# Performance work log

Measured on AMD Instinct MI355X. Metric: run time of the kernel, lower is better.

Reference implementation:

```python
import jax, jax.numpy as jnp
import numpy as np

# NF4 codebook (16 values, as in bitsandbytes / torchao), block size 64
NF4_CODEBOOK = jnp.array([
    -1.0, -0.6961928009986877, -0.5250730514526367, -0.39491748809814453,
    -0.28444138169288635, -0.18477343022823334, -0.09105003625154495, 0.0,
    0.07958029955625534, 0.16093020141124725, 0.24611230194568634,
    0.33791524171829224, 0.44070982933044434, 0.5626170039176941,
    0.7229568362236023, 1.0], dtype=jnp.float32)
BLOCK = 64
IN_DIM, OUT_DIM, RANK, ALPHA = 4096, 4096, 16, 32.0
N_TOKENS = 8192


def setup_inputs() -> dict:
    key = jax.random.key(0)
    kw, kx, ka, kb = jax.random.split(key, 4)
    # full-precision weight, then NF4-quantize (per-block absmax scaler + nearest code)
    w = jax.random.normal(kw, (OUT_DIM, IN_DIM), dtype=jnp.float32) * 0.02
    blocks = w.reshape(-1, BLOCK)                                   # [n_blocks, 64]
    scalers = jnp.max(jnp.abs(blocks), axis=1) + 1e-12              # [n_blocks]
    normed = blocks / scalers[:, None]
    codes = jnp.argmin(jnp.abs(normed[:, :, None] - NF4_CODEBOOK[None, None, :]),
                       axis=-1).astype(jnp.int32)                   # [n_blocks, 64]
    x = jax.random.normal(kx, (N_TOKENS, IN_DIM), dtype=jnp.float32)
    # kaiming_uniform_(a=sqrt(5)) -> U(-1/sqrt(fan_in), 1/sqrt(fan_in))
    bound_a = 1.0 / np.sqrt(IN_DIM)
    bound_b = 1.0 / np.sqrt(RANK)
    lora_a_w = jax.random.uniform(ka, (RANK, IN_DIM), minval=-bound_a, maxval=bound_a, dtype=jnp.float32)
    lora_b_w = jax.random.uniform(kb, (OUT_DIM, RANK), minval=-bound_b, maxval=bound_b, dtype=jnp.float32)
    return {"x": x, "codes": codes, "scalers": scalers,
            "lora_a_w": lora_a_w, "lora_b_w": lora_b_w}


def reference(x, codes, scalers, lora_a_w, lora_b_w):
    in_dim = x.shape[-1]
    out_dim = (codes.shape[0] * codes.shape[1]) // in_dim
    # NF4 dequant: code -> codebook value, times per-block absmax scaler
    w = (NF4_CODEBOOK[codes] * scalers[:, None]).reshape(out_dim, in_dim)
    base = x @ w.T                                                  # [N, out_dim]
    # LoRA branch (dropout p=0.0 -> identity): (alpha/rank) * B(A(x))
    lora = (x @ lora_a_w.T) @ lora_b_w.T
    return base + (ALPHA / RANK) * lora
```

## Files before the change

kernel.cpp:

```cpp
#include <hip/hip_runtime.h>

#define IN_DIM 4096
#define OUT_DIM 4096
#define NTOK 8192
#define LORA_SCALE 2.0f

typedef __bf16 bf16x8 __attribute__((ext_vector_type(8)));
typedef float f32x4 __attribute__((ext_vector_type(4)));

__device__ __constant__ float NF4_CB[16] = {
    -1.0f, -0.6961928009986877f, -0.5250730514526367f, -0.39491748809814453f,
    -0.28444138169288635f, -0.18477343022823334f, -0.09105003625154495f, 0.0f,
    0.07958029955625534f, 0.16093020141124725f, 0.24611230194568634f,
    0.33791524171829224f, 0.44070982933044434f, 0.5626170039176941f,
    0.7229568362236023f, 1.0f};

#define GLOAD16(g, l)                                                         \
  __builtin_amdgcn_global_load_lds(                                           \
      (const __attribute__((address_space(1))) void*)(g),                     \
      (__attribute__((address_space(3))) void*)(l), 16, 0, 0)

#define WEFF2_BLOCKS (OUT_DIM / 8 * (IN_DIM / 2048))
#define XCVT_BLOCKS (NTOK * IN_DIM / (256 * 8))

__global__ __launch_bounds__(256) void prep_kernel(
    const float* __restrict__ x, const int* __restrict__ codes,
    const float* __restrict__ scalers, const float* __restrict__ la,
    const float* __restrict__ lb, __bf16* __restrict__ xb,
    __bf16* __restrict__ weff) {
  if (blockIdx.x < WEFF2_BLOCKS) {
    const int lane = threadIdx.x & 63;
    const float cbv = NF4_CB[lane & 15];
    const int o0 = (blockIdx.x >> 1) * 8;
    const int k = ((blockIdx.x & 1) << 11) + threadIdx.x * 8;
    float4 a[16][2];
#pragma unroll
    for (int r = 0; r < 16; ++r) {
      a[r][0] = *(const float4*)(la + r * IN_DIM + k);
      a[r][1] = *(const float4*)(la + r * IN_DIM + k + 4);
    }
#pragma unroll 1
    for (int rr = 0; rr < 8; ++rr) {
      const int o = o0 + rr;
      const size_t base = (size_t)o * IN_DIM + k;
      const float sc = scalers[base >> 6];
      const int4 c0 = *(const int4*)(codes + base);
      const int4 c1 = *(const int4*)(codes + base + 4);
      float v[8];
      v[0] = __shfl(cbv, c0.x, 64) * sc; v[1] = __shfl(cbv, c0.y, 64) * sc;
      v[2] = __shfl(cbv, c0.z, 64) * sc; v[3] = __shfl(cbv, c0.w, 64) * sc;
      v[4] = __shfl(cbv, c1.x, 64) * sc; v[5] = __shfl(cbv, c1.y, 64) * sc;
      v[6] = __shfl(cbv, c1.z, 64) * sc; v[7] = __shfl(cbv, c1.w, 64) * sc;
      const float* lbo = lb + o * 16;
#pragma unroll
      for (int r = 0; r < 16; ++r) {
        float br = LORA_SCALE * lbo[r];
        v[0] += br * a[r][0].x; v[1] += br * a[r][0].y;
        v[2] += br * a[r][0].z; v[3] += br * a[r][0].w;
        v[4] += br * a[r][1].x; v[5] += br * a[r][1].y;
        v[6] += br * a[r][1].z; v[7] += br * a[r][1].w;
      }
      union { __bf16 h[8]; int4 i4; } u;
#pragma unroll
      for (int t = 0; t < 8; ++t) u.h[t] = (__bf16)v[t];
      *(int4*)(weff + base) = u.i4;
    }
  } else {
    size_t g = ((size_t)(blockIdx.x - WEFF2_BLOCKS) * 256 + threadIdx.x) * 8;
    const float4 a = *(const float4*)(x + g);
    const float4 b = *(const float4*)(x + g + 4);
    union { __bf16 h[8]; int4 i4; } u;
    u.h[0] = (__bf16)a.x; u.h[1] = (__bf16)a.y;
    u.h[2] = (__bf16)a.z; u.h[3] = (__bf16)a.w;
    u.h[4] = (__bf16)b.x; u.h[5] = (__bf16)b.y;
    u.h[6] = (__bf16)b.z; u.h[7] = (__bf16)b.w;
    *(int4*)(xb + g) = u.i4;
  }
}

#define BAR() asm volatile("s_barrier" ::: "memory")
#define WAITV6() asm volatile("s_waitcnt vmcnt(6)" ::: "memory")
#define WAITV0() asm volatile("s_waitcnt vmcnt(0)" ::: "memory")

__global__ __launch_bounds__(512, 2) void gemm_bt_kernel(
    const __bf16* __restrict__ A,
    const __bf16* __restrict__ B,
    float* __restrict__ C) {
  const int K = IN_DIM;
  const int N = OUT_DIM;
  __shared__ __align__(16) char lds[131072];

  const int lin = blockIdx.x;
  const int swz = (lin & 7) * 64 + (lin >> 3);
  const int m0 = (swz >> 4) * 256;
  const int n0 = (swz & 15) * 256;

  const int tid = threadIdx.x;
  const int w = tid >> 6;
  const int l = tid & 63;
  const int wr = w >> 2;
  const int wc = w & 3;

  const int kxor = (((l >> 4) * 16) ^ ((l & 7) << 4));
  const int offA = (wr * 64 + (l & 15)) * 128 + kxor;
  const int offB = (wc * 32 + (l & 15)) * 128 + kxor;

  const int lr0 = w * 8 + (l >> 3);
  const int scol = ((l & 7) ^ (l >> 3)) * 8;
  const __bf16* gA[2][2];
  const __bf16* gB[2][2];
#pragma unroll
  for (int r = 0; r < 2; ++r)
#pragma unroll
    for (int s = 0; s < 2; ++s) {
      const int lrs = lr0 + s * 64;
      gA[r][s] = A + (size_t)(m0 + (lrs >> 6) * 128 + r * 64 + (lrs & 63)) * K + scol;
      gB[r][s] = B + (size_t)(n0 + (lrs >> 5) * 64 + r * 32 + (lrs & 31)) * K + scol;
    }

#define STAGE_A(b, r, kt)                                   \
  do {                                                      \
    char* d_ = lds + ((b)*2 + (r)) * 16384 + w * 1024;      \
    GLOAD16(gA[r][0] + (kt), d_);                           \
    GLOAD16(gA[r][1] + (kt), d_ + 8192);                    \
  } while (0)
#define STAGE_B(b, r, kt)                                          \
  do {                                                             \
    char* d_ = lds + 65536 + ((b)*2 + (r)) * 16384 + w * 1024;     \
    GLOAD16(gB[r][0] + (kt), d_);                                  \
    GLOAD16(gB[r][1] + (kt), d_ + 8192);                           \
  } while (0)

#define LDA(b, r, i, ks) \
  (*(const bf16x8*)(lds + ((b)*2 + (r)) * 16384 + (offA ^ ((ks)*64)) + (i)*2048))
#define LDB(b, r, j, ks) \
  (*(const bf16x8*)(lds + 65536 + ((b)*2 + (r)) * 16384 + (offB ^ ((ks)*64)) + (j)*2048))

  f32x4 acc[8][4] = {};
  bf16x8 af[4][2], bf[2][2];

#define QUAD(I0, J0)                                                          \
  do {                                                                        \
    __builtin_amdgcn_s_setprio(1);                                            \
    _Pragma("unroll") for (int i = 0; i < 4; ++i)                             \
        _Pragma("unroll") for (int j = 0; j < 2; ++j) {                       \
      acc[(I0) + i][(J0) + j] = __builtin_amdgcn_mfma_f32_16x16x32_bf16(      \
          af[i][0], bf[j][0], acc[(I0) + i][(J0) + j], 0, 0, 0);              \
      acc[(I0) + i][(J0) + j] = __builtin_amdgcn_mfma_f32_16x16x32_bf16(      \
          af[i][1], bf[j][1], acc[(I0) + i][(J0) + j], 0, 0, 0);              \
    }                                                                         \
    __builtin_amdgcn_s_setprio(0);                                            \
  } while (0)

#define TILE(b, S0, KT1, S2, KT2, VM)                                         \
  do {                                                                        \
    _Pragma("unroll") for (int i = 0; i < 4; ++i) {                           \
      af[i][0] = LDA(b, 0, i, 0); af[i][1] = LDA(b, 0, i, 1);                 \
    }                                                                         \
    _Pragma("unroll") for (int j = 0; j < 2; ++j) {                           \
      bf[j][0] = LDB(b, 0, j, 0); bf[j][1] = LDB(b, 0, j, 1);                 \
    }                                                                         \
    if (S0) STAGE_B(1 - (b), 0, KT1);                                         \
    BAR(); QUAD(0, 0); BAR();                                                 \
    _Pragma("unroll") for (int j = 0; j < 2; ++j) {                           \
      bf[j][0] = LDB(b, 1, j, 0); bf[j][1] = LDB(b, 1, j, 1);                 \
    }                                                                         \
    if (S2) STAGE_A(b, 0, KT2);                                               \
    BAR(); QUAD(0, 2); BAR();                                                 \
    _Pragma("unroll") for (int i = 0; i < 4; ++i) {                           \
      af[i][0] = LDA(b, 1, i, 0); af[i][1] = LDA(b, 1, i, 1);                 \
    }                                                                         \
    if (S2) STAGE_B(b, 1, KT2);                                               \
    BAR(); QUAD(4, 2); BAR();                                                 \
    _Pragma("unroll") for (int j = 0; j < 2; ++j) {                           \
      bf[j][0] = LDB(b, 0, j, 0); bf[j][1] = LDB(b, 0, j, 1);                 \
    }                                                                         \
    if (S2) STAGE_A(b, 1, KT2);                                               \
    BAR(); QUAD(4, 0); VM; BAR();                                             \
  } while (0)

  STAGE_A(0, 0, 0); STAGE_B(0, 0, 0); STAGE_B(0, 1, 0); STAGE_A(0, 1, 0);
  STAGE_A(1, 0, 64); STAGE_B(1, 1, 64); STAGE_A(1, 1, 64);
  WAITV6();
  BAR();

#pragma unroll 1
  for (int t = 0; t < 62; t += 2) {
    const int kt1 = (t + 1) * 64;
    const int kt2 = (t + 2) * 64;
    const int kt3 = (t + 3) * 64;
    TILE(0, true, kt1, true, kt2, WAITV6());
    TILE(1, true, kt2, true, kt3, WAITV6());
  }
  TILE(0, true, 63 * 64, false, 0, WAITV0());
  TILE(1, false, 0, false, 0, ((void)0));

  const int er = m0 + wr * 128 + 4 * (l >> 4);
  const int ec = n0 + wc * 64 + (l & 15);
#pragma unroll
  for (int i = 0; i < 8; ++i)
#pragma unroll
    for (int j = 0; j < 4; ++j)
#pragma unroll
      for (int rr = 0; rr < 4; ++rr)
        C[(size_t)(er + i * 16 + rr) * N + ec + j * 16] = acc[i][j][rr];
}

extern "C" void kernel_launch(void* const* d_in, const int* in_sizes, int n_in,
                              void* d_out, int out_size, void* d_ws,
                              size_t ws_size, hipStream_t stream) {
  const float* x = (const float*)d_in[0];
  const int* codes = (const int*)d_in[1];
  const float* scalers = (const float*)d_in[2];
  const float* la = (const float*)d_in[3];
  const float* lb = (const float*)d_in[4];
  float* out = (float*)d_out;

  __bf16* xb = (__bf16*)d_ws;
  __bf16* weff = (__bf16*)((char*)d_ws + (size_t)NTOK * IN_DIM * 2);

  prep_kernel<<<WEFF2_BLOCKS + XCVT_BLOCKS, 256, 0, stream>>>(
      x, codes, scalers, la, lb, xb, weff);
  gemm_bt_kernel<<<(NTOK / 256) * (OUT_DIM / 256), 512, 0, stream>>>(xb, weff,
                                                                     out);
}
```

Baseline: 486.7 us.

## Compute LoRA branch in fp32 epilogue instead of folding into bf16 weight

Before, the LoRA update B·A was folded into the dequantized weight before rounding to bf16. Now the prep kernel computes x·A^T in fp32 (scaled) while converting x to bf16, and the weight is plain NF4 dequant. The GEMM epilogue loads the xa and LB tiles into LDS and adds the rank-16 product in fp32 before storing C. This keeps the LoRA term at higher precision and removes the 16-FMA-per-element fold from weight prep. In exchange the xa rows need a reduction over the full input dimension and the GEMM epilogue gains extra LDS traffic and FMAs.

```diff
diff --git a/kernel.cpp b/kernel.cpp
--- a/kernel.cpp
+++ b/kernel.cpp
@@ -6,6 +6,7 @@
 #define LORA_SCALE 2.0f
 
 typedef __bf16 bf16x8 __attribute__((ext_vector_type(8)));
+typedef __bf16 bf16x4 __attribute__((ext_vector_type(4)));
 typedef float f32x4 __attribute__((ext_vector_type(4)));
 
 __device__ __constant__ float NF4_CB[16] = {
@@ -20,61 +21,78 @@
       (const __attribute__((address_space(1))) void*)(g),                     \
       (__attribute__((address_space(3))) void*)(l), 16, 0, 0)
 
-#define WEFF2_BLOCKS (OUT_DIM / 8 * (IN_DIM / 2048))
-#define XCVT_BLOCKS (NTOK * IN_DIM / (256 * 8))
+#define XA_BLOCKS (NTOK / 16)
+#define WEFF_BLOCKS (OUT_DIM * IN_DIM / (256 * 8))
 
 __global__ __launch_bounds__(256) void prep_kernel(
     const float* __restrict__ x, const int* __restrict__ codes,
     const float* __restrict__ scalers, const float* __restrict__ la,
-    const float* __restrict__ lb, __bf16* __restrict__ xb,
-    __bf16* __restrict__ weff) {
-  if (blockIdx.x < WEFF2_BLOCKS) {
+    __bf16* __restrict__ xb, __bf16* __restrict__ weff,
+    float* __restrict__ xa) {
+  if (blockIdx.x < XA_BLOCKS) {
+    const int l = threadIdx.x & 63;
+    const int w = threadIdx.x >> 6;
+    const int row0 = blockIdx.x * 16 + w * 4;
+    float acc[4][16] = {};
+#pragma unroll 1
+    for (int i = 0; i < 16; ++i) {
+      const int k = i * 256 + l * 4;
+      float4 xv[4];
+#pragma unroll
+      for (int j = 0; j < 4; ++j)
+        xv[j] = *(const float4*)(x + (size_t)(row0 + j) * IN_DIM + k);
+#pragma unroll
+      for (int j = 0; j < 4; ++j) {
+        bf16x4 h;
+        h[0] = (__bf16)xv[j].x; h[1] = (__bf16)xv[j].y;
+        h[2] = (__bf16)xv[j].z; h[3] = (__bf16)xv[j].w;
+        *(bf16x4*)(xb + (size_t)(row0 + j) * IN_DIM + k) = h;
+      }
+#pragma unroll
+      for (int r = 0; r < 16; ++r) {
+        const float4 av = *(const float4*)(la + r * IN_DIM + k);
+#pragma unroll
+        for (int j = 0; j < 4; ++j) {
+          acc[j][r] += xv[j].x * av.x; acc[j][r] += xv[j].y * av.y;
+          acc[j][r] += xv[j].z * av.z; acc[j][r] += xv[j].w * av.w;
+        }
+      }
+    }
+#pragma unroll
+    for (int j = 0; j < 4; ++j)
+#pragma unroll
+      for (int r = 0; r < 16; ++r) {
+        float v = acc[j][r];
+        v += __shfl_xor(v, 1);  v += __shfl_xor(v, 2);
+        v += __shfl_xor(v, 4);  v += __shfl_xor(v, 8);
+        v += __shfl_xor(v, 16); v += __shfl_xor(v, 32);
+        acc[j][r] = v;
+      }
+    if (l == 0) {
+#pragma unroll
+      for (int j = 0; j < 4; ++j)
+#pragma unroll
+        for (int r = 0; r < 16; ++r)
+          xa[(size_t)(row0 + j) * 16 + r] = LORA_SCALE * acc[j][r];
+    }
+  } else {
     const int lane = threadIdx.x & 63;
     const float cbv = NF4_CB[lane & 15];
-    const int o0 = (blockIdx.x >> 1) * 8;
-    const int k = ((blockIdx.x & 1) << 11) + threadIdx.x * 8;
-    float4 a[16][2];
-#pragma unroll
-    for (int r = 0; r < 16; ++r) {
-      a[r][0] = *(const float4*)(la + r * IN_DIM + k);
-      a[r][1] = *(const float4*)(la + r * IN_DIM + k + 4);
-    }
-#pragma unroll 1
-    for (int rr = 0; rr < 8; ++rr) {
-      const int o = o0 + rr;
-      const size_t base = (size_t)o * IN_DIM + k;
-      const float sc = scalers[base >> 6];
-      const int4 c0 = *(const int4*)(codes + base);
-      const int4 c1 = *(const int4*)(codes + base + 4);
-      float v[8];
-      v[0] = __shfl(cbv, c0.x, 64) * sc; v[1] = __shfl(cbv, c0.y, 64) * sc;
-      v[2] = __shfl(cbv, c0.z, 64) * sc; v[3] = __shfl(cbv, c0.w, 64) * sc;
-      v[4] = __shfl(cbv, c1.x, 64) * sc; v[5] = __shfl(cbv, c1.y, 64) * sc;
-      v[6] = __shfl(cbv, c1.z, 64) * sc; v[7] = __shfl(cbv, c1.w, 64) * sc;
-      const float* lbo = lb + o * 16;
-#pragma unroll
-      for (int r = 0; r < 16; ++r) {
-        float br = LORA_SCALE * lbo[r];
-        v[0] += br * a[r][0].x; v[1] += br * a[r][0].y;
-        v[2] += br * a[r][0].z; v[3] += br * a[r][0].w;
-        v[4] += br * a[r][1].x; v[5] += br * a[r][1].y;
-        v[6] += br * a[r][1].z; v[7] += br * a[r][1].w;
-      }
-      union { __bf16 h[8]; int4 i4; } u;
-#pragma unroll
-      for (int t = 0; t < 8; ++t) u.h[t] = (__bf16)v[t];
-      *(int4*)(weff + base) = u.i4;
-    }
-  } else {
-    size_t g = ((size_t)(blockIdx.x - WEFF2_BLOCKS) * 256 + threadIdx.x) * 8;
-    const float4 a = *(const float4*)(x + g);
-    const float4 b = *(const float4*)(x + g + 4);
+    const size_t base =
+        ((size_t)(blockIdx.x - XA_BLOCKS) * 256 + threadIdx.x) * 8;
+    const float sc = scalers[base >> 6];
+    const int4 c0 = *(const int4*)(codes + base);
+    const int4 c1 = *(const int4*)(codes + base + 4);
     union { __bf16 h[8]; int4 i4; } u;
-    u.h[0] = (__bf16)a.x; u.h[1] = (__bf16)a.y;
-    u.h[2] = (__bf16)a.z; u.h[3] = (__bf16)a.w;
-    u.h[4] = (__bf16)b.x; u.h[5] = (__bf16)b.y;
-    u.h[6] = (__bf16)b.z; u.h[7] = (__bf16)b.w;
-    *(int4*)(xb + g) = u.i4;
+    u.h[0] = (__bf16)(__shfl(cbv, c0.x, 64) * sc);
+    u.h[1] = (__bf16)(__shfl(cbv, c0.y, 64) * sc);
+    u.h[2] = (__bf16)(__shfl(cbv, c0.z, 64) * sc);
+    u.h[3] = (__bf16)(__shfl(cbv, c0.w, 64) * sc);
+    u.h[4] = (__bf16)(__shfl(cbv, c1.x, 64) * sc);
+    u.h[5] = (__bf16)(__shfl(cbv, c1.y, 64) * sc);
+    u.h[6] = (__bf16)(__shfl(cbv, c1.z, 64) * sc);
+    u.h[7] = (__bf16)(__shfl(cbv, c1.w, 64) * sc);
+    *(int4*)(weff + base) = u.i4;
   }
 }
 
@@ -85,6 +103,8 @@
 __global__ __launch_bounds__(512, 2) void gemm_bt_kernel(
     const __bf16* __restrict__ A,
     const __bf16* __restrict__ B,
+    const float* __restrict__ XA,
+    const float* __restrict__ LB,
     float* __restrict__ C) {
   const int K = IN_DIM;
   const int N = OUT_DIM;
@@ -195,15 +215,49 @@
   TILE(0, true, 63 * 64, false, 0, WAITV0());
   TILE(1, false, 0, false, 0, ((void)0));
 
+  float* xa_s = (float*)lds;
+  float* lb_s = (float*)(lds + 16384);
+  {
+    const float4* xg = (const float4*)(XA + (size_t)m0 * 16);
+    const float4* lg = (const float4*)(LB + (size_t)n0 * 16);
+    ((float4*)xa_s)[tid] = xg[tid];
+    ((float4*)xa_s)[tid + 512] = xg[tid + 512];
+    ((float4*)lb_s)[tid] = lg[tid];
+    ((float4*)lb_s)[tid + 512] = lg[tid + 512];
+  }
+  __syncthreads();
+
+  f32x4 lbf[4][4];
+#pragma unroll
+  for (int j = 0; j < 4; ++j) {
+    const int lc = wc * 64 + (l & 15) + j * 16;
+#pragma unroll
+    for (int q = 0; q < 4; ++q)
+      lbf[j][q] = *(const f32x4*)(lb_s + lc * 16 + q * 4);
+  }
+
   const int er = m0 + wr * 128 + 4 * (l >> 4);
   const int ec = n0 + wc * 64 + (l & 15);
 #pragma unroll
   for (int i = 0; i < 8; ++i)
 #pragma unroll
-    for (int j = 0; j < 4; ++j)
-#pragma unroll
-      for (int rr = 0; rr < 4; ++rr)
-        C[(size_t)(er + i * 16 + rr) * N + ec + j * 16] = acc[i][j][rr];
+    for (int rr = 0; rr < 4; ++rr) {
+      const int lr = wr * 128 + 4 * (l >> 4) + i * 16 + rr;
+      f32x4 xv[4];
+#pragma unroll
+      for (int q = 0; q < 4; ++q)
+        xv[q] = *(const f32x4*)(xa_s + lr * 16 + q * 4);
+#pragma unroll
+      for (int j = 0; j < 4; ++j) {
+        float s = 0.f;
+#pragma unroll
+        for (int q = 0; q < 4; ++q) {
+          s += xv[q][0] * lbf[j][q][0]; s += xv[q][1] * lbf[j][q][1];
+          s += xv[q][2] * lbf[j][q][2]; s += xv[q][3] * lbf[j][q][3];
+        }
+        C[(size_t)(er + i * 16 + rr) * N + ec + j * 16] = acc[i][j][rr] + s;
+      }
+    }
 }
 
 extern "C" void kernel_launch(void* const* d_in, const int* in_sizes, int n_in,
@@ -218,9 +272,11 @@
 
   __bf16* xb = (__bf16*)d_ws;
   __bf16* weff = (__bf16*)((char*)d_ws + (size_t)NTOK * IN_DIM * 2);
-
-  prep_kernel<<<WEFF2_BLOCKS + XCVT_BLOCKS, 256, 0, stream>>>(
-      x, codes, scalers, la, lb, xb, weff);
-  gemm_bt_kernel<<<(NTOK / 256) * (OUT_DIM / 256), 512, 0, stream>>>(xb, weff,
-                                                                     out);
+  float* xa = (float*)((char*)d_ws + (size_t)NTOK * IN_DIM * 2 +
+                       (size_t)OUT_DIM * IN_DIM * 2);
+
+  prep_kernel<<<XA_BLOCKS + WEFF_BLOCKS, 256, 0, stream>>>(
+      x, codes, scalers, la, xb, weff, xa);
+  gemm_bt_kernel<<<(NTOK / 256) * (OUT_DIM / 256), 512, 0, stream>>>(
+      xb, weff, xa, lb, out);
 }
```

Result: slower. 536.1 us (+10.1%).
